# Kernel optimization log

Measured on AMD Instinct MI355X. Metric: run time of the kernel, lower is better.

## Reference

```python
import jax, jax.numpy as jnp
import numpy as np

C = 640      # in_channels == out_channels (required by source: same generator applied to both)
K = 3        # kernel_size
R = int(C * 0.2)  # reduction hidden = 128
H = 10
W = 10
BS = 25      # support: 5-way 5-shot
BQ = 75      # query: 5-way 15-query


def setup_inputs() -> dict:
    key = jax.random.key(0)
    ks = jax.random.split(key, 16)
    s = 0.02  # weight scale to keep the 4-deep linear chain numerically tame
    rn = lambda k, shape: jax.random.normal(k, shape, jnp.float32) * s
    return {
        "support_set": jax.random.normal(ks[0], (BS, C, H, W), jnp.float32),
        "query_set": jax.random.normal(ks[1], (BQ, C, H, W), jnp.float32),
        # ContextLearningModule: four 1x1 convs (no nonlinearity in source)
        "Wc1": rn(ks[2], (C, C)), "bc1": jnp.zeros((C,), jnp.float32),
        "Wc2": rn(ks[3], (C, C)), "bc2": jnp.zeros((C,), jnp.float32),
        "Wc3": rn(ks[4], (C, C)), "bc3": jnp.zeros((C,), jnp.float32),
        "Wc4": rn(ks[5], (C, C)), "bc4": jnp.zeros((C,), jnp.float32),
        # DynamicKernelGenerator channel branch: Linear(C,R) -> ReLU -> Linear(R, C*K*K)
        "W1": rn(ks[6], (C, R)), "b1": jnp.zeros((R,), jnp.float32),
        "W2": rn(ks[7], (R, C * K * K)), "b2": jnp.zeros((C * K * K,), jnp.float32),
        # DynamicKernelGenerator spatial branch: Conv2d(C, K*K, 1)
        "Ws": rn(ks[8], (K * K, C)), "bs": jnp.zeros((K * K,), jnp.float32),
    }


def _conv1x1(x, Wt, b):
    # x: [b, c, h, w], Wt: [o, c]
    return jnp.einsum('bchw,oc->bohw', x, Wt) + b[None, :, None, None]


def _dyn_kernel(x, W1, b1, W2, b2, Ws, bs):
    # x: [b, C, h, w] -> per-pixel dynamic kernel [b, C, h, w, K, K]
    b, c, h, w = x.shape
    pooled = x.mean(axis=(2, 3))  # adaptive_avg_pool2d(...,1)
    ck = jax.nn.relu(pooled @ W1 + b1) @ W2 + b2          # [b, C*K*K]
    ck = ck.reshape(b, c, K, K)                            # channel kernel
    sk = jnp.einsum('bchw,kc->bkhw', x, Ws) + bs[None, :, None, None]
    sk = sk.reshape(b, h, w, K, K)                         # raw view, as in source
    return ck[:, :, None, None, :, :] * sk[:, None, :, :, :, :]


def _involution(x, kernel):
    # x: [b, C, h, w]; kernel: [b or 1, C, h, w, K, K]
    # out[b,c,i,j] = sum_{u,v} kernel[b,c,i,j,u,v] * x[b,c,i+u-p, j+v-p]
    h, w = x.shape[-2:]
    p = K // 2
    xp = jnp.pad(x, ((0, 0), (0, 0), (p, p), (p, p)))
    return sum(kernel[..., u, v] * xp[:, :, u:u + h, v:v + w]
               for u in range(K) for v in range(K))


def reference(support_set, query_set, Wc1, bc1, Wc2, bc2, Wc3, bc3, Wc4, bc4,
              W1, b1, W2, b2, Ws, bs):
    sf, qf = support_set, query_set  # identity backbone
    # context learning module
    tsr = _conv1x1(_conv1x1(_conv1x1(_conv1x1(sf, Wc1, bc1), Wc2, bc2), Wc3, bc3), Wc4, bc4)
    # task-specific kernel, averaged over the support batch -> [1, C, H, W, K, K]
    task_kernel = _dyn_kernel(tsr, W1, b1, W2, b2, Ws, bs).mean(axis=0, keepdims=True)
    # per-instance kernels (batched; identical math to the per-sample loop)
    inst_kernels = _dyn_kernel(sf, W1, b1, W2, b2, Ws, bs)  # [BS, C, H, W, K, K]
    fused = inst_kernels * task_kernel
    adapted_support = _involution(sf, fused)        # [BS, C, H, W]
    adapted_query = _involution(qf, task_kernel)    # [BQ, C, H, W] (kernel broadcast)
    return (adapted_support, adapted_query)
```

## Files before the change

kernel.cpp:

```cpp
#include <hip/hip_runtime.h>

#define CCH   640
#define RDIM  128
#define HWPIX 100
#define NBS   25
#define NBQ   75
#define CKK   5760
#define SF_B  64000

#define OFF_PG0   0
#define OFF_PGA   16000
#define OFF_PGB   32000
#define OFF_ATA   48000
#define OFF_ATB   53760
#define OFF_BA    59520
#define OFF_BB    59536
#define OFF_HP    59552
#define OFF_SKT   85152
#define OFF_SKS   130152
#define OFF_SKSCT 175152
#define OFF_CKT   197652
#define OFF_CKS   341652
#define OFF_TASKT 485652

__global__ void pool_kernel(const float* __restrict__ sf, float* __restrict__ Pg0) {
    int idx = blockIdx.x * 64 + threadIdx.x;
    if (idx >= NBS * CCH) return;
    int b = idx / CCH, c = idx % CCH;
    const float4* s4 = (const float4*)(sf + b * SF_B + c * HWPIX);
    float acc = 0.f;
#pragma unroll
    for (int q = 0; q < 25; ++q) {
        float4 v = s4[q];
        acc += (v.x + v.y) + (v.z + v.w);
    }
    Pg0[idx] = acc * 0.01f;
}

__global__ void chain_step(const float* __restrict__ Pin, const float* __restrict__ Wp,
                           const float* __restrict__ bp, float* __restrict__ Pout,
                           const float* __restrict__ Ain, const float* __restrict__ Wa,
                           const float* __restrict__ ba, const float* __restrict__ Bin,
                           float* __restrict__ Aout, float* __restrict__ Bout,
                           int first, const float* __restrict__ Ws, const float* __restrict__ bs) {
    __shared__ float red[256];
    int blk = blockIdx.x, t = threadIdx.x;
    int lane = t & 63;
    if (blk < 4000) {
        int W = blk * 4 + (t >> 6);
        int o = W / NBS, b = W % NBS;
        const float2* w2 = (const float2*)(Wp + o * CCH);
        const float2* p2 = (const float2*)(Pin + b * CCH);
        float acc = 0.f;
#pragma unroll
        for (int s = 0; s < 5; ++s) {
            float2 wv = w2[s * 64 + lane];
            float2 pv = p2[s * 64 + lane];
            acc += wv.x * pv.x + wv.y * pv.y;
        }
#pragma unroll
        for (int m = 32; m >= 1; m >>= 1) acc += __shfl_xor(acc, m);
        if (lane == 0) Pout[b * CCH + o] = acc + bp[o];
    } else if (blk < 4090) {
        int w = blk - 4000;
        int k = w / 10, ctile = w % 10;
        int og = t >> 6, cl = lane;
        int c = ctile * 64 + cl;
        int o0 = og * 160;
        float acc = 0.f;
        if (first) {
            const float* ar = Ws + k * CCH;
#pragma unroll 8
            for (int o = o0; o < o0 + 160; ++o)
                acc += ar[o] * Wa[o * CCH + c];
        } else {
#pragma unroll 8
            for (int o = o0; o < o0 + 160; ++o)
                acc += Ain[o * 9 + k] * Wa[o * CCH + c];
        }
        red[t] = acc;
        __syncthreads();
        if (t < 64) {
            float s = red[t] + red[64 + t] + red[128 + t] + red[192 + t];
            Aout[(ctile * 64 + t) * 9 + k] = s;
        }
    } else {
        int WB = (blk - 4090) * 4 + (t >> 6);
        if (WB >= 9) return;
        int k = WB;
        float acc = 0.f;
        if (first) {
            const float* ar = Ws + k * CCH;
#pragma unroll
            for (int s = 0; s < 10; ++s) acc += ar[s * 64 + lane] * ba[s * 64 + lane];
        } else {
#pragma unroll
            for (int s = 0; s < 10; ++s) acc += Ain[(s * 64 + lane) * 9 + k] * ba[s * 64 + lane];
        }
#pragma unroll
        for (int m = 32; m >= 1; m >>= 1) acc += __shfl_xor(acc, m);
        if (lane == 0) Bout[k] = acc + (first ? bs[k] : Bin[k]);
    }
}

__global__ void postchain(const float* __restrict__ sf, const float* __restrict__ Pg0,
                          const float* __restrict__ Pgf, const float* __restrict__ W1,
                          float* __restrict__ Hp, const float* __restrict__ A4T,
                          const float* __restrict__ betaF, const float* __restrict__ Ws,
                          const float* __restrict__ bs, float* __restrict__ SKT,
                          float* __restrict__ SKS) {
    int blk = blockIdx.x, t = threadIdx.x;
    if (blk < 100) {
        int pair = blk / 2;
        int s = (blk % 2) * 2 + (t >> 7);
        int r = t & 127;
        int branch = pair / NBS, b = pair % NBS;
        const float* prow = (branch ? Pg0 : Pgf) + b * CCH;
        int c0 = s * 160;
        float acc = 0.f;
#pragma unroll 8
        for (int c = 0; c < 160; ++c)
            acc += prow[c0 + c] * W1[(c0 + c) * RDIM + r];
        Hp[(pair * 4 + s) * RDIM + r] = acc;
    } else {
        int sidx = (blk - 100) * 256 + t;
        if (sidx >= 45000) return;
        int s = sidx / 22500;
        int rem = sidx % 22500;
        int b = rem / 900;
        int r2 = rem % 900;
        int k = r2 / HWPIX, q = r2 % HWPIX;
        const float* x = sf + b * SF_B + q;
        const float* wsr = Ws + k * CCH;
        int c0 = s * 320;
        float acc0 = 0.f, acc1 = 0.f;
#pragma unroll 8
        for (int c = 0; c < 320; ++c) {
            float xc = x[(c0 + c) * HWPIX];
            acc0 += A4T[(c0 + c) * 9 + k] * xc;
            acc1 += wsr[c0 + c] * xc;
        }
        if (s == 0) { acc0 += betaF[k]; acc1 += bs[k]; }
        int p = r2 / 9, uv = r2 % 9;
        int dst = s * 22500 + b * 900 + uv * 100 + p;
        SKT[dst] = acc0;
        SKS[dst] = acc1;
    }
}

__global__ void mlp_phase2(const float* __restrict__ Hp, const float* __restrict__ b1,
                           const float* __restrict__ W2, const float* __restrict__ b2,
                           float* __restrict__ ckt, float* __restrict__ cks) {
    __shared__ float hs0[RDIM], hs1[RDIM];
    int b = blockIdx.x / 9, chunk = blockIdx.x % 9;
    int t = threadIdx.x;
    if (t < RDIM) {
        const float* hp = Hp + b * 4 * RDIM;
        hs0[t] = fmaxf(b1[t] + hp[t] + hp[RDIM + t] + hp[2 * RDIM + t] + hp[3 * RDIM + t], 0.f);
    } else if (t < 2 * RDIM) {
        int r = t - RDIM;
        const float* hp = Hp + (NBS + b) * 4 * RDIM;
        hs1[r] = fmaxf(b1[r] + hp[r] + hp[RDIM + r] + hp[2 * RDIM + r] + hp[3 * RDIM + r], 0.f);
    }
    __syncthreads();
    int jbase = chunk * 640;
    float a00 = b2[jbase + t], a01 = b2[jbase + t + 320];
    float a10 = a00, a11 = a01;
#pragma unroll 4
    for (int r = 0; r < RDIM; ++r) {
        const float* wrow = W2 + r * CKK + jbase;
        float w0 = wrow[t], w1 = wrow[t + 320];
        float h0 = hs0[r], h1 = hs1[r];
        a00 += h0 * w0; a01 += h0 * w1;
        a10 += h1 * w0; a11 += h1 * w1;
    }
    float* c0 = ckt + b * CKK + jbase;
    float* c1 = cks + b * CKK + jbase;
    c0[t] = a00; c0[t + 320] = a01;
    c1[t] = a10; c1[t + 320] = a11;
}

__global__ void task_assemble(const float* __restrict__ ckt, const float* __restrict__ SKT,
                              const float* __restrict__ SKS, float* __restrict__ taskT,
                              float* __restrict__ sksT) {
    int blk = blockIdx.x, t = threadIdx.x;
    if (blk < 2250) {
        int idx = blk * 256 + t;
        int uv = idx / 64000;
        int rem = idx % 64000;
        int c = rem / 100, p = rem % 100;
        float acc = 0.f;
#pragma unroll
        for (int b = 0; b < NBS; ++b)
            acc += ckt[b * CKK + c * 9 + uv] *
                   (SKT[b * 900 + uv * 100 + p] + SKT[22500 + b * 900 + uv * 100 + p]);
        taskT[idx] = acc * 0.04f;
    } else {
        int cidx = (blk - 2250) * 256 + t;
        if (cidx >= 22500) return;
        int uv = cidx / 2500;
        int r = cidx % 2500;
        int src = (r / 100) * 900 + uv * 100 + (r % 100);
        sksT[cidx] = SKS[src] + SKS[22500 + src];
    }
}

__global__ __launch_bounds__(256) void involutions(
        const float* __restrict__ sf, const float* __restrict__ qf,
        const float* __restrict__ taskT, const float* __restrict__ cks,
        const float* __restrict__ sksT, float* __restrict__ out) {
    int idx = blockIdx.x * 256 + threadIdx.x;
    bool support = idx < NBS * SF_B;
    int b, c, p;
    const float* x;
    if (support) {
        b = idx / SF_B; int rem = idx % SF_B; c = rem / 100; p = rem % 100;
        x = sf + b * SF_B + c * 100;
    } else {
        int qidx = idx - NBS * SF_B;
        b = qidx / SF_B; int rem = qidx % SF_B; c = rem / 100; p = rem % 100;
        x = qf + b * SF_B + c * 100;
    }
    int i = p / 10, j = p % 10;
    float acc = 0.f;
#pragma unroll
    for (int u = 0; u < 3; ++u) {
        int ii = i + u - 1;
        float mrow = ((unsigned)ii < 10u) ? 1.f : 0.f;
        int ci = min(max(ii, 0), 9);
#pragma unroll
        for (int v = 0; v < 3; ++v) {
            int jj = j + v - 1;
            float m = ((unsigned)jj < 10u) ? mrow : 0.f;
            int cj = min(max(jj, 0), 9);
            float xv = x[ci * 10 + cj] * m;
            int uv = u * 3 + v;
            float w = taskT[uv * 64000 + c * 100 + p];
            if (support)
                w *= cks[b * CKK + c * 9 + uv] * sksT[uv * 2500 + b * 100 + p];
            acc += w * xv;
        }
    }
    out[idx] = acc;
}

extern "C" void kernel_launch(void* const* d_in, const int* in_sizes, int n_in,
                              void* d_out, int out_size, void* d_ws, size_t ws_size,
                              hipStream_t stream) {
    const float* sf  = (const float*)d_in[0];
    const float* qf  = (const float*)d_in[1];
    const float* Wc[4] = {(const float*)d_in[2], (const float*)d_in[4],
                          (const float*)d_in[6], (const float*)d_in[8]};
    const float* bc[4] = {(const float*)d_in[3], (const float*)d_in[5],
                          (const float*)d_in[7], (const float*)d_in[9]};
    const float* W1 = (const float*)d_in[10];
    const float* b1 = (const float*)d_in[11];
    const float* W2 = (const float*)d_in[12];
    const float* b2 = (const float*)d_in[13];
    const float* Ws = (const float*)d_in[14];
    const float* bs = (const float*)d_in[15];
    float* out = (float*)d_out;
    float* ws = (float*)d_ws;

    float* Pg0 = ws + OFF_PG0;
    float* Pga = ws + OFF_PGA;
    float* Pgb = ws + OFF_PGB;
    float* ATa = ws + OFF_ATA;
    float* ATb = ws + OFF_ATB;
    float* Ba  = ws + OFF_BA;
    float* Bb  = ws + OFF_BB;
    float* Hp  = ws + OFF_HP;
    float* SKT = ws + OFF_SKT;
    float* SKS = ws + OFF_SKS;
    float* SKsT= ws + OFF_SKSCT;
    float* CKT = ws + OFF_CKT;
    float* CKS = ws + OFF_CKS;
    float* TKT = ws + OFF_TASKT;

    pool_kernel<<<250, 64, 0, stream>>>(sf, Pg0);

    chain_step<<<4093, 256, 0, stream>>>(Pg0, Wc[0], bc[0], Pga, nullptr, Wc[3], bc[3], nullptr,
                                         ATa, Ba, 1, Ws, bs);
    chain_step<<<4093, 256, 0, stream>>>(Pga, Wc[1], bc[1], Pgb, ATa, Wc[2], bc[2], Ba,
                                         ATb, Bb, 0, Ws, bs);
    chain_step<<<4093, 256, 0, stream>>>(Pgb, Wc[2], bc[2], Pga, ATb, Wc[1], bc[1], Bb,
                                         ATa, Ba, 0, Ws, bs);
    chain_step<<<4093, 256, 0, stream>>>(Pga, Wc[3], bc[3], Pgb, ATa, Wc[0], bc[0], Ba,
                                         ATb, Bb, 0, Ws, bs);

    postchain<<<276, 256, 0, stream>>>(sf, Pg0, Pgb, W1, Hp, ATb, Bb, Ws, bs, SKT, SKS);
    mlp_phase2<<<225, 320, 0, stream>>>(Hp, b1, W2, b2, CKT, CKS);
    task_assemble<<<2338, 256, 0, stream>>>(CKT, SKT, SKS, TKT, SKsT);
    involutions<<<25000, 256, 0, stream>>>(sf, qf, TKT, CKS, SKsT, out);
}
```

Measured before the change: 231.3 us.

## Fuse pooling, context chain and MLP into one per-sample prelude kernel

Replaces the pool, four chain_step launches, postchain and mlp_phase2 with a single 34-block prelude kernel. Each block handles one support sample end to end in shared memory, or one spatial-kernel row propagated backwards through the conv chain. The spatial-kernel kernel no longer splits its channel reduction in two and writes SKS directly in the layout the involution kernel reads. This removes several launches and intermediate global round trips, but runs the chain and MLP on only 34 large blocks, which limits parallelism and puts much more serial work on each block.

```diff
diff --git a/kernel.cpp b/kernel.cpp
--- a/kernel.cpp
+++ b/kernel.cpp
@@ -8,201 +8,168 @@
 #define CKK   5760
 #define SF_B  64000
 
-#define OFF_PG0   0
-#define OFF_PGA   16000
-#define OFF_PGB   32000
-#define OFF_ATA   48000
-#define OFF_ATB   53760
-#define OFF_BA    59520
-#define OFF_BB    59536
-#define OFF_HP    59552
-#define OFF_SKT   85152
-#define OFF_SKS   130152
-#define OFF_SKSCT 175152
-#define OFF_CKT   197652
-#define OFF_CKS   341652
-#define OFF_TASKT 485652
-
-__global__ void pool_kernel(const float* __restrict__ sf, float* __restrict__ Pg0) {
-    int idx = blockIdx.x * 64 + threadIdx.x;
-    if (idx >= NBS * CCH) return;
-    int b = idx / CCH, c = idx % CCH;
-    const float4* s4 = (const float4*)(sf + b * SF_B + c * HWPIX);
+#define OFF_A4T   0
+#define OFF_BETA  5760
+#define OFF_CKT   5776
+#define OFF_CKS   149776
+#define OFF_SKT   293776
+#define OFF_SKS   316276
+#define OFF_TASKT 338776
+
+__global__ __launch_bounds__(1024) void prelude(
+        const float* __restrict__ sf,
+        const float* __restrict__ Wc0, const float* __restrict__ bc0,
+        const float* __restrict__ Wc1, const float* __restrict__ bc1,
+        const float* __restrict__ Wc2, const float* __restrict__ bc2,
+        const float* __restrict__ Wc3, const float* __restrict__ bc3,
+        const float* __restrict__ W1,  const float* __restrict__ b1,
+        const float* __restrict__ W2,  const float* __restrict__ b2,
+        const float* __restrict__ Ws,  const float* __restrict__ bs,
+        float* __restrict__ CKT, float* __restrict__ CKS,
+        float* __restrict__ A4T, float* __restrict__ Beta) {
+    __shared__ float p0[CCH], pa[CCH], pb[CCH];
+    __shared__ float hpart[8][RDIM];
+    __shared__ float hs[2][RDIM];
+    __shared__ float red[1024];
+    __shared__ float betaS;
+
+    const float* Wcf[4] = {Wc0, Wc1, Wc2, Wc3};
+    const float* bcf[4] = {bc0, bc1, bc2, bc3};
+
+    int blk = blockIdx.x, t = threadIdx.x;
+    int wv = t >> 6, lane = t & 63;
+
+    if (blk < NBS) {
+        int b = blk;
+        if (t < CCH) {
+            const float4* s4 = (const float4*)(sf + b * SF_B + t * HWPIX);
+            float acc = 0.f;
+#pragma unroll
+            for (int q = 0; q < 25; ++q) {
+                float4 v = s4[q];
+                acc += (v.x + v.y) + (v.z + v.w);
+            }
+            float pv = acc * 0.01f;
+            p0[t] = pv;
+            pa[t] = pv;
+        }
+        __syncthreads();
+        for (int s = 0; s < 4; ++s) {
+            const float* W = Wcf[s];
+            const float* bias = bcf[s];
+            float* pin  = (s & 1) ? pb : pa;
+            float* pout = (s & 1) ? pa : pb;
+#pragma unroll 2
+            for (int g = 0; g < 40; ++g) {
+                int o = g * 16 + wv;
+                const float* wrow = W + o * CCH;
+                float acc = 0.f;
+#pragma unroll
+                for (int s5 = 0; s5 < 10; ++s5)
+                    acc += wrow[s5 * 64 + lane] * pin[s5 * 64 + lane];
+#pragma unroll
+                for (int m = 32; m >= 1; m >>= 1) acc += __shfl_xor(acc, m);
+                if (lane == 0) pout[o] = acc + bias[o];
+            }
+            __syncthreads();
+        }
+        {
+            int r = t & 127, sl = (t >> 7) & 3, br = t >> 9;
+            const float* pv = br ? p0 : pa;
+            int c0 = sl * 160;
+            float acc = 0.f;
+#pragma unroll 8
+            for (int c = 0; c < 160; ++c)
+                acc += pv[c0 + c] * W1[(c0 + c) * RDIM + r];
+            hpart[br * 4 + sl][r] = acc;
+        }
+        __syncthreads();
+        if (t < 256) {
+            int br = t >> 7, r = t & 127;
+            hs[br][r] = fmaxf(b1[r] + hpart[br * 4][r] + hpart[br * 4 + 1][r]
+                              + hpart[br * 4 + 2][r] + hpart[br * 4 + 3][r], 0.f);
+        }
+        __syncthreads();
+        for (int j = t; j < CKK; j += 1024) {
+            float a0 = b2[j], a1 = a0;
+#pragma unroll 8
+            for (int r = 0; r < RDIM; ++r) {
+                float wvv = W2[r * CKK + j];
+                a0 += hs[0][r] * wvv;
+                a1 += hs[1][r] * wvv;
+            }
+            CKT[b * CKK + j] = a0;
+            CKS[b * CKK + j] = a1;
+        }
+    } else {
+        int k = blk - NBS;
+        const float* WcR[4] = {Wc3, Wc2, Wc1, Wc0};
+        const float* bcR[4] = {bc3, bc2, bc1, bc0};
+        if (t < CCH) pa[t] = Ws[k * CCH + t];
+        if (t == 0) betaS = bs[k];
+        __syncthreads();
+        for (int s = 0; s < 4; ++s) {
+            const float* W = WcR[s];
+            const float* bcv = bcR[s];
+            float* pin  = (s & 1) ? pb : pa;
+            float* pout = (s & 1) ? pa : pb;
+            red[t] = (t < CCH) ? pin[t] * bcv[t] : 0.f;
+            float acc = 0.f;
+            if (t < CCH) {
+#pragma unroll 8
+                for (int o = 0; o < CCH; ++o)
+                    acc += pin[o] * W[o * CCH + t];
+            }
+            __syncthreads();
+            if (t < 64) {
+                float ssum = 0.f;
+#pragma unroll
+                for (int m = 0; m < 16; ++m) ssum += red[m * 64 + t];
+#pragma unroll
+                for (int mm = 32; mm >= 1; mm >>= 1) ssum += __shfl_xor(ssum, mm);
+                if (t == 0) betaS += ssum;
+            }
+            if (t < CCH) pout[t] = acc;
+            __syncthreads();
+        }
+        if (t < CCH) A4T[t * 9 + k] = pa[t];
+        if (t == 0) Beta[k] = betaS;
+    }
+}
+
+__global__ void sk_both(const float* __restrict__ sf, const float* __restrict__ A4T,
+                        const float* __restrict__ Beta, const float* __restrict__ Ws,
+                        const float* __restrict__ bs, float* __restrict__ SKT,
+                        float* __restrict__ SKS) {
+    int idx = blockIdx.x * 256 + threadIdx.x;
+    if (idx >= NBS * 900) return;
+    int b = idx / 900, r2 = idx % 900;
+    int k = r2 / HWPIX, q = r2 % HWPIX;
+    const float* x = sf + b * SF_B + q;
+    const float* wsr = Ws + k * CCH;
+    float a0 = Beta[k], a1 = bs[k];
+#pragma unroll 8
+    for (int c = 0; c < CCH; ++c) {
+        float xc = x[c * HWPIX];
+        a0 += A4T[c * 9 + k] * xc;
+        a1 += wsr[c] * xc;
+    }
+    int p = r2 / 9, uv = r2 % 9;
+    SKT[b * 900 + uv * 100 + p] = a0;
+    SKS[uv * 2500 + b * 100 + p] = a1;
+}
+
+__global__ void task_assemble(const float* __restrict__ CKT, const float* __restrict__ SKT,
+                              float* __restrict__ taskT) {
+    int idx = blockIdx.x * 256 + threadIdx.x;
+    int uv = idx / 64000;
+    int rem = idx % 64000;
+    int c = rem / 100, p = rem % 100;
     float acc = 0.f;
 #pragma unroll
-    for (int q = 0; q < 25; ++q) {
-        float4 v = s4[q];
-        acc += (v.x + v.y) + (v.z + v.w);
-    }
-    Pg0[idx] = acc * 0.01f;
-}
-
-__global__ void chain_step(const float* __restrict__ Pin, const float* __restrict__ Wp,
-                           const float* __restrict__ bp, float* __restrict__ Pout,
-                           const float* __restrict__ Ain, const float* __restrict__ Wa,
-                           const float* __restrict__ ba, const float* __restrict__ Bin,
-                           float* __restrict__ Aout, float* __restrict__ Bout,
-                           int first, const float* __restrict__ Ws, const float* __restrict__ bs) {
-    __shared__ float red[256];
-    int blk = blockIdx.x, t = threadIdx.x;
-    int lane = t & 63;
-    if (blk < 4000) {
-        int W = blk * 4 + (t >> 6);
-        int o = W / NBS, b = W % NBS;
-        const float2* w2 = (const float2*)(Wp + o * CCH);
-        const float2* p2 = (const float2*)(Pin + b * CCH);
-        float acc = 0.f;
-#pragma unroll
-        for (int s = 0; s < 5; ++s) {
-            float2 wv = w2[s * 64 + lane];
-            float2 pv = p2[s * 64 + lane];
-            acc += wv.x * pv.x + wv.y * pv.y;
-        }
-#pragma unroll
-        for (int m = 32; m >= 1; m >>= 1) acc += __shfl_xor(acc, m);
-        if (lane == 0) Pout[b * CCH + o] = acc + bp[o];
-    } else if (blk < 4090) {
-        int w = blk - 4000;
-        int k = w / 10, ctile = w % 10;
-        int og = t >> 6, cl = lane;
-        int c = ctile * 64 + cl;
-        int o0 = og * 160;
-        float acc = 0.f;
-        if (first) {
-            const float* ar = Ws + k * CCH;
-#pragma unroll 8
-            for (int o = o0; o < o0 + 160; ++o)
-                acc += ar[o] * Wa[o * CCH + c];
-        } else {
-#pragma unroll 8
-            for (int o = o0; o < o0 + 160; ++o)
-                acc += Ain[o * 9 + k] * Wa[o * CCH + c];
-        }
-        red[t] = acc;
-        __syncthreads();
-        if (t < 64) {
-            float s = red[t] + red[64 + t] + red[128 + t] + red[192 + t];
-            Aout[(ctile * 64 + t) * 9 + k] = s;
-        }
-    } else {
-        int WB = (blk - 4090) * 4 + (t >> 6);
-        if (WB >= 9) return;
-        int k = WB;
-        float acc = 0.f;
-        if (first) {
-            const float* ar = Ws + k * CCH;
-#pragma unroll
-            for (int s = 0; s < 10; ++s) acc += ar[s * 64 + lane] * ba[s * 64 + lane];
-        } else {
-#pragma unroll
-            for (int s = 0; s < 10; ++s) acc += Ain[(s * 64 + lane) * 9 + k] * ba[s * 64 + lane];
-        }
-#pragma unroll
-        for (int m = 32; m >= 1; m >>= 1) acc += __shfl_xor(acc, m);
-        if (lane == 0) Bout[k] = acc + (first ? bs[k] : Bin[k]);
-    }
-}
-
-__global__ void postchain(const float* __restrict__ sf, const float* __restrict__ Pg0,
-                          const float* __restrict__ Pgf, const float* __restrict__ W1,
-                          float* __restrict__ Hp, const float* __restrict__ A4T,
-                          const float* __restrict__ betaF, const float* __restrict__ Ws,
-                          const float* __restrict__ bs, float* __restrict__ SKT,
-                          float* __restrict__ SKS) {
-    int blk = blockIdx.x, t = threadIdx.x;
-    if (blk < 100) {
-        int pair = blk / 2;
-        int s = (blk % 2) * 2 + (t >> 7);
-        int r = t & 127;
-        int branch = pair / NBS, b = pair % NBS;
-        const float* prow = (branch ? Pg0 : Pgf) + b * CCH;
-        int c0 = s * 160;
-        float acc = 0.f;
-#pragma unroll 8
-        for (int c = 0; c < 160; ++c)
-            acc += prow[c0 + c] * W1[(c0 + c) * RDIM + r];
-        Hp[(pair * 4 + s) * RDIM + r] = acc;
-    } else {
-        int sidx = (blk - 100) * 256 + t;
-        if (sidx >= 45000) return;
-        int s = sidx / 22500;
-        int rem = sidx % 22500;
-        int b = rem / 900;
-        int r2 = rem % 900;
-        int k = r2 / HWPIX, q = r2 % HWPIX;
-        const float* x = sf + b * SF_B + q;
-        const float* wsr = Ws + k * CCH;
-        int c0 = s * 320;
-        float acc0 = 0.f, acc1 = 0.f;
-#pragma unroll 8
-        for (int c = 0; c < 320; ++c) {
-            float xc = x[(c0 + c) * HWPIX];
-            acc0 += A4T[(c0 + c) * 9 + k] * xc;
-            acc1 += wsr[c0 + c] * xc;
-        }
-        if (s == 0) { acc0 += betaF[k]; acc1 += bs[k]; }
-        int p = r2 / 9, uv = r2 % 9;
-        int dst = s * 22500 + b * 900 + uv * 100 + p;
-        SKT[dst] = acc0;
-        SKS[dst] = acc1;
-    }
-}
-
-__global__ void mlp_phase2(const float* __restrict__ Hp, const float* __restrict__ b1,
-                           const float* __restrict__ W2, const float* __restrict__ b2,
-                           float* __restrict__ ckt, float* __restrict__ cks) {
-    __shared__ float hs0[RDIM], hs1[RDIM];
-    int b = blockIdx.x / 9, chunk = blockIdx.x % 9;
-    int t = threadIdx.x;
-    if (t < RDIM) {
-        const float* hp = Hp + b * 4 * RDIM;
-        hs0[t] = fmaxf(b1[t] + hp[t] + hp[RDIM + t] + hp[2 * RDIM + t] + hp[3 * RDIM + t], 0.f);
-    } else if (t < 2 * RDIM) {
-        int r = t - RDIM;
-        const float* hp = Hp + (NBS + b) * 4 * RDIM;
-        hs1[r] = fmaxf(b1[r] + hp[r] + hp[RDIM + r] + hp[2 * RDIM + r] + hp[3 * RDIM + r], 0.f);
-    }
-    __syncthreads();
-    int jbase = chunk * 640;
-    float a00 = b2[jbase + t], a01 = b2[jbase + t + 320];
-    float a10 = a00, a11 = a01;
-#pragma unroll 4
-    for (int r = 0; r < RDIM; ++r) {
-        const float* wrow = W2 + r * CKK + jbase;
-        float w0 = wrow[t], w1 = wrow[t + 320];
-        float h0 = hs0[r], h1 = hs1[r];
-        a00 += h0 * w0; a01 += h0 * w1;
-        a10 += h1 * w0; a11 += h1 * w1;
-    }
-    float* c0 = ckt + b * CKK + jbase;
-    float* c1 = cks + b * CKK + jbase;
-    c0[t] = a00; c0[t + 320] = a01;
-    c1[t] = a10; c1[t + 320] = a11;
-}
-
-__global__ void task_assemble(const float* __restrict__ ckt, const float* __restrict__ SKT,
-                              const float* __restrict__ SKS, float* __restrict__ taskT,
-                              float* __restrict__ sksT) {
-    int blk = blockIdx.x, t = threadIdx.x;
-    if (blk < 2250) {
-        int idx = blk * 256 + t;
-        int uv = idx / 64000;
-        int rem = idx % 64000;
-        int c = rem / 100, p = rem % 100;
-        float acc = 0.f;
-#pragma unroll
-        for (int b = 0; b < NBS; ++b)
-            acc += ckt[b * CKK + c * 9 + uv] *
-                   (SKT[b * 900 + uv * 100 + p] + SKT[22500 + b * 900 + uv * 100 + p]);
-        taskT[idx] = acc * 0.04f;
-    } else {
-        int cidx = (blk - 2250) * 256 + t;
-        if (cidx >= 22500) return;
-        int uv = cidx / 2500;
-        int r = cidx % 2500;
-        int src = (r / 100) * 900 + uv * 100 + (r % 100);
-        sksT[cidx] = SKS[src] + SKS[22500 + src];
-    }
+    for (int b = 0; b < NBS; ++b)
+        acc += CKT[b * CKK + c * 9 + uv] * SKT[b * 900 + uv * 100 + p];
+    taskT[idx] = acc * 0.04f;
 }
 
 __global__ __launch_bounds__(256) void involutions(
@@ -249,10 +216,14 @@
                               hipStream_t stream) {
     const float* sf  = (const float*)d_in[0];
     const float* qf  = (const float*)d_in[1];
-    const float* Wc[4] = {(const float*)d_in[2], (const float*)d_in[4],
-                          (const float*)d_in[6], (const float*)d_in[8]};
-    const float* bc[4] = {(const float*)d_in[3], (const float*)d_in[5],
-                          (const float*)d_in[7], (const float*)d_in[9]};
+    const float* Wc0 = (const float*)d_in[2];
+    const float* bc0 = (const float*)d_in[3];
+    const float* Wc1 = (const float*)d_in[4];
+    const float* bc1 = (const float*)d_in[5];
+    const float* Wc2 = (const float*)d_in[6];
+    const float* bc2 = (const float*)d_in[7];
+    const float* Wc3 = (const float*)d_in[8];
+    const float* bc3 = (const float*)d_in[9];
     const float* W1 = (const float*)d_in[10];
     const float* b1 = (const float*)d_in[11];
     const float* W2 = (const float*)d_in[12];
@@ -262,34 +233,17 @@
     float* out = (float*)d_out;
     float* ws = (float*)d_ws;
 
-    float* Pg0 = ws + OFF_PG0;
-    float* Pga = ws + OFF_PGA;
-    float* Pgb = ws + OFF_PGB;
-    float* ATa = ws + OFF_ATA;
-    float* ATb = ws + OFF_ATB;
-    float* Ba  = ws + OFF_BA;
-    float* Bb  = ws + OFF_BB;
-    float* Hp  = ws + OFF_HP;
+    float* A4T = ws + OFF_A4T;
+    float* Bet = ws + OFF_BETA;
+    float* CKT = ws + OFF_CKT;
+    float* CKS = ws + OFF_CKS;
     float* SKT = ws + OFF_SKT;
     float* SKS = ws + OFF_SKS;
-    float* SKsT= ws + OFF_SKSCT;
-    float* CKT = ws + OFF_CKT;
-    float* CKS = ws + OFF_CKS;
     float* TKT = ws + OFF_TASKT;
 
-    pool_kernel<<<250, 64, 0, stream>>>(sf, Pg0);
-
-    chain_step<<<4093, 256, 0, stream>>>(Pg0, Wc[0], bc[0], Pga, nullptr, Wc[3], bc[3], nullptr,
-                                         ATa, Ba, 1, Ws, bs);
-    chain_step<<<4093, 256, 0, stream>>>(Pga, Wc[1], bc[1], Pgb, ATa, Wc[2], bc[2], Ba,
-                                         ATb, Bb, 0, Ws, bs);
-    chain_step<<<4093, 256, 0, stream>>>(Pgb, Wc[2], bc[2], Pga, ATb, Wc[1], bc[1], Bb,
-                                         ATa, Ba, 0, Ws, bs);
-    chain_step<<<4093, 256, 0, stream>>>(Pga, Wc[3], bc[3], Pgb, ATa, Wc[0], bc[0], Ba,
-                                         ATb, Bb, 0, Ws, bs);
-
-    postchain<<<276, 256, 0, stream>>>(sf, Pg0, Pgb, W1, Hp, ATb, Bb, Ws, bs, SKT, SKS);
-    mlp_phase2<<<225, 320, 0, stream>>>(Hp, b1, W2, b2, CKT, CKS);
-    task_assemble<<<2338, 256, 0, stream>>>(CKT, SKT, SKS, TKT, SKsT);
-    involutions<<<25000, 256, 0, stream>>>(sf, qf, TKT, CKS, SKsT, out);
-}
+    prelude<<<34, 1024, 0, stream>>>(sf, Wc0, bc0, Wc1, bc1, Wc2, bc2, Wc3, bc3,
+                                     W1, b1, W2, b2, Ws, bs, CKT, CKS, A4T, Bet);
+    sk_both<<<88, 256, 0, stream>>>(sf, A4T, Bet, Ws, bs, SKT, SKS);
+    task_assemble<<<2250, 256, 0, stream>>>(CKT, SKT, TKT);
+    involutions<<<25000, 256, 0, stream>>>(sf, qf, TKT, CKS, SKS, out);
+}
```

After: 348.9 us. 1.51x slower.
